# Performance work log

Measured on AMD Instinct MI355X. Metric: run time of the kernel, lower is better.

Reference implementation:

```python
import jax, jax.numpy as jnp
import numpy as np

TAU_MEM, TAU_SYN = 20.0, 5.0
THRESHOLD, BETA, RESET = 1.0, 4.0, 0.0
ALPHA_MEM = float(np.exp(-1.0 / TAU_MEM))
ALPHA_SYN = float(np.exp(-1.0 / TAU_SYN))
EPS = 1e-6


def _lif(x, W, b):
    # x: [B,T,D] -> spikes_with_grad: [B,T,H] (faithful to original incl. the
    # spikes + stop_grad(spikes - surrogate) expression, forward value 2*s - sg)
    cur = jnp.einsum('btd,dh->bth', x, W) + b  # all-timestep projection (same math as per-step dense)
    B, T, H = cur.shape
    v0 = jnp.zeros((B, H), cur.dtype)
    i0 = jnp.zeros((B, H), cur.dtype)

    def step(carry, ic):
        v, i = carry
        i = ALPHA_SYN * i + ic
        v = ALPHA_MEM * v + (1.0 - ALPHA_MEM) * i
        spikes = (v >= THRESHOLD).astype(jnp.float32)
        sg = BETA / (2.0 * (1.0 + jnp.cosh(BETA * (v - THRESHOLD))))
        swg = spikes + jax.lax.stop_gradient(spikes - sg)
        v = jnp.where(spikes > 0, RESET, v)
        return (v, i), swg

    (_, _), out = jax.lax.scan(step, (v0, i0), cur.transpose(1, 0, 2))
    return out.transpose(1, 0, 2)


def _layernorm(x, scale, bias):
    mu = jnp.mean(x, axis=-1, keepdims=True)
    var = jnp.var(x, axis=-1, keepdims=True)
    return (x - mu) * jax.lax.rsqrt(var + EPS) * scale + bias


def setup_inputs() -> dict:
    key = jax.random.key(0)
    ks = jax.random.split(key, 8)
    B, T, D = 512, 128, 512
    H0, H1, H2, C = 256, 128, 64, 2
    s = 0.02
    return {
        'spike_trains': jax.random.uniform(ks[0], (B, T, D), jnp.float32),
        'W0': jax.random.normal(ks[1], (D, H0), jnp.float32) * s,
        'b0': jnp.zeros((H0,), jnp.float32),
        'ln1_scale': jnp.ones((H0,), jnp.float32),
        'ln1_bias': jnp.zeros((H0,), jnp.float32),
        'W1': jax.random.normal(ks[2], (H0, H1), jnp.float32) * s,
        'b1': jnp.zeros((H1,), jnp.float32),
        'ln2_scale': jnp.ones((H1,), jnp.float32),
        'ln2_bias': jnp.zeros((H1,), jnp.float32),
        'W2': jax.random.normal(ks[3], (H1, H2), jnp.float32) * s,
        'b2': jnp.zeros((H2,), jnp.float32),
        'Wc': jax.random.normal(ks[4], (H2, C), jnp.float32) * s,
        'bc': jnp.zeros((C,), jnp.float32),
    }


def reference(spike_trains, W0, b0, ln1_scale, ln1_bias, W1, b1,
              ln2_scale, ln2_bias, W2, b2, Wc, bc):
    x = _lif(spike_trains, W0, b0)                    # layer 0: no pre-norm
    x = _lif(_layernorm(x, ln1_scale, ln1_bias), W1, b1)
    x = _lif(_layernorm(x, ln2_scale, ln2_bias), W2, b2)
    pooled = jnp.mean(x, axis=1)                      # [B, H2]
    logits = pooled @ Wc + bc                         # [B, C]
    return logits, pooled, jnp.mean(x)
```

## Files before the change

kernel.cpp:

```cpp
#include <hip/hip_runtime.h>
#include <cstddef>

static constexpr float A_MEM  = 0.951229424500714f;
static constexpr float A_SYN  = 0.8187307530779818f;
static constexpr float OM_MEM = 0.04877057549928599f;

template<int NT, int K, int H, bool LN, bool POOL>
__global__ __launch_bounds__(NT) void layer_fused(
    const float* __restrict__ A, const float* __restrict__ W,
    const float* __restrict__ bias,
    const float* __restrict__ lns, const float* __restrict__ lnb,
    float* __restrict__ out)
{
  constexpr int T = 128;
  constexpr int BK = 16;
  constexpr int TXB = (NT == 512) ? 5 : 4;
  constexpr int NTX = 1 << TXB;
  constexpr int NJ  = H / NTX;
  constexpr int S   = K / BK;
  constexpr int APT = (BK * 128 / 4) / NT;
  constexpr int WPT = (BK * H / 4) / NT < 1 ? 1 : (BK * H / 4) / NT;
  extern __shared__ __align__(16) float smem[];
  float* As  = smem;
  float* Ws  = smem + BK * 128;
  float* buf = smem;

  const int b   = blockIdx.x;
  const int tid = threadIdx.x;
  const int tx  = tid & (NTX - 1);
  const int ty  = tid >> TXB;
  const float* Ab = A + (size_t)b * T * K;

  float acc[8][NJ];
  #pragma unroll
  for (int i = 0; i < 8; ++i)
    #pragma unroll
    for (int j = 0; j < NJ; ++j) acc[i][j] = 0.f;

  float4 aR[APT], wR[WPT];
  auto load_tile = [&](int k0) {
    #pragma unroll
    for (int p = 0; p < APT; ++p) {
      int f4 = tid + p * NT;
      int r  = f4 >> 2;
      int c4 = (f4 & 3) << 2;
      aR[p] = *(const float4*)(Ab + (size_t)r * K + k0 + c4);
    }
    #pragma unroll
    for (int p = 0; p < WPT; ++p) {
      int f4 = tid + p * NT;
      int k  = f4 / (H / 4);
      int c4 = (f4 % (H / 4)) << 2;
      wR[p] = *(const float4*)(W + (size_t)(k0 + k) * H + c4);
    }
  };

  load_tile(0);
  for (int s = 0; s < S; ++s) {
    __syncthreads();
    #pragma unroll
    for (int p = 0; p < APT; ++p) {
      int f4 = tid + p * NT;
      int r  = f4 >> 2;
      int c4 = (f4 & 3) << 2;
      As[(c4 + 0) * 128 + r] = aR[p].x;
      As[(c4 + 1) * 128 + r] = aR[p].y;
      As[(c4 + 2) * 128 + r] = aR[p].z;
      As[(c4 + 3) * 128 + r] = aR[p].w;
    }
    #pragma unroll
    for (int p = 0; p < WPT; ++p) {
      int f4 = tid + p * NT;
      int k  = f4 / (H / 4);
      int c4 = (f4 % (H / 4)) << 2;
      *(float4*)(Ws + k * H + c4) = wR[p];
    }
    __syncthreads();
    if (s + 1 < S) load_tile((s + 1) * BK);
    #pragma unroll
    for (int kk = 0; kk < BK; ++kk) {
      float4 a0 = *(const float4*)(As + kk * 128 + ty * 8);
      float4 a1 = *(const float4*)(As + kk * 128 + ty * 8 + 4);
      float av[8] = {a0.x, a0.y, a0.z, a0.w, a1.x, a1.y, a1.z, a1.w};
      float bv[NJ];
      #pragma unroll
      for (int j = 0; j < NJ; ++j) bv[j] = Ws[kk * H + j * NTX + tx];
      #pragma unroll
      for (int i = 0; i < 8; ++i)
        #pragma unroll
        for (int j = 0; j < NJ; ++j)
          acc[i][j] += av[i] * bv[j];
    }
  }

  __syncthreads();
  {
    float bb[NJ];
    #pragma unroll
    for (int j = 0; j < NJ; ++j) bb[j] = bias[j * NTX + tx];
    #pragma unroll
    for (int i = 0; i < 8; ++i) {
      int row = ty * 8 + i;
      #pragma unroll
      for (int j = 0; j < NJ; ++j)
        buf[row * H + j * NTX + tx] = acc[i][j] + bb[j];
    }
  }
  __syncthreads();

  if (tid < H) {
    float v = 0.f, cin = 0.f, sum = 0.f;
    for (int t = 0; t < T; ++t) {
      float ic = buf[t * H + tid];
      cin = A_SYN * cin + ic;
      v = A_MEM * v + OM_MEM * cin;
      bool sp = (v >= 1.0f);
      float xx = 4.0f * (v - 1.0f);
      float e  = __expf(xx);
      float tp = 1.0f + e;
      float sg = 4.0f * e / (tp * tp);
      float o  = (sp ? 2.0f : 0.0f) - sg;
      if (POOL) sum += o;
      else buf[t * H + tid] = o;
      v = sp ? 0.0f : v;
    }
    if (POOL) out[(size_t)b * H + tid] = sum * (1.0f / 128.0f);
  }

  if (LN) {
    __syncthreads();
    constexpr int VPL = H / 64;
    constexpr int NW  = NT / 64;
    const int wv   = tid >> 6;
    const int lane = tid & 63;
    float sc[VPL], bi[VPL];
    #pragma unroll
    for (int q = 0; q < VPL; ++q) {
      sc[q] = lns[lane * VPL + q];
      bi[q] = lnb[lane * VPL + q];
    }
    for (int t = wv; t < T; t += NW) {
      float vals[VPL];
      #pragma unroll
      for (int q = 0; q < VPL; ++q) vals[q] = buf[t * H + lane * VPL + q];
      float s1 = 0.f, s2 = 0.f;
      #pragma unroll
      for (int q = 0; q < VPL; ++q) { s1 += vals[q]; s2 += vals[q] * vals[q]; }
      #pragma unroll
      for (int off = 32; off; off >>= 1) {
        s1 += __shfl_xor(s1, off);
        s2 += __shfl_xor(s2, off);
      }
      float mu  = s1 * (1.0f / H);
      float var = s2 * (1.0f / H) - mu * mu;
      float rs  = rsqrtf(var + 1e-6f);
      float* op = out + ((size_t)b * T + t) * H + lane * VPL;
      #pragma unroll
      for (int q = 0; q < VPL; ++q)
        op[q] = (vals[q] - mu) * rs * sc[q] + bi[q];
    }
  }
}

__global__ __launch_bounds__(1024) void head_k(
    const float* __restrict__ pooled, const float* __restrict__ Wc,
    const float* __restrict__ bc, float* __restrict__ logits,
    float* __restrict__ meanp)
{
    const int tid = threadIdx.x;
    const int b = tid >> 1, c = tid & 1;
    float accl = 0.f;
    #pragma unroll 8
    for (int k = 0; k < 64; ++k) accl += pooled[b * 64 + k] * Wc[k * 2 + c];
    logits[tid] = accl + bc[c];

    float s = 0.f;
    for (int i2 = tid; i2 < 512 * 64; i2 += 1024) s += pooled[i2];
    #pragma unroll
    for (int off = 32; off; off >>= 1) s += __shfl_xor(s, off);
    __shared__ float red[16];
    const int wave = tid >> 6, lane = tid & 63;
    if (lane == 0) red[wave] = s;
    __syncthreads();
    if (tid == 0) {
        float tot = 0.f;
        #pragma unroll
        for (int w = 0; w < 16; ++w) tot += red[w];
        meanp[0] = tot * (1.0f / 32768.0f);
    }
}

extern "C" void kernel_launch(void* const* d_in, const int* in_sizes, int n_in,
                              void* d_out, int out_size, void* d_ws, size_t ws_size,
                              hipStream_t stream) {
    const float* x    = (const float*)d_in[0];
    const float* W0   = (const float*)d_in[1];
    const float* b0   = (const float*)d_in[2];
    const float* ln1s = (const float*)d_in[3];
    const float* ln1b = (const float*)d_in[4];
    const float* W1   = (const float*)d_in[5];
    const float* b1   = (const float*)d_in[6];
    const float* ln2s = (const float*)d_in[7];
    const float* ln2b = (const float*)d_in[8];
    const float* W2   = (const float*)d_in[9];
    const float* b2   = (const float*)d_in[10];
    const float* Wc   = (const float*)d_in[11];
    const float* bc   = (const float*)d_in[12];

    float* out    = (float*)d_out;
    float* logits = out;
    float* pooled = out + 1024;
    float* meanp  = out + 1024 + 32768;

    const int B = 512;
    float* y1 = (float*)d_ws;
    float* y2 = y1 + (size_t)65536 * 256;

    (void)hipFuncSetAttribute((const void*)&layer_fused<512,512,256,true,false>,
                              hipFuncAttributeMaxDynamicSharedMemorySize, 131072);
    (void)hipFuncSetAttribute((const void*)&layer_fused<256,256,128,true,false>,
                              hipFuncAttributeMaxDynamicSharedMemorySize, 65536);
    (void)hipFuncSetAttribute((const void*)&layer_fused<256,128,64,false,true>,
                              hipFuncAttributeMaxDynamicSharedMemorySize, 32768);

    layer_fused<512,512,256,true,false><<<B, 512, 131072, stream>>>(
        x,  W0, b0, ln1s, ln1b, y1);
    layer_fused<256,256,128,true,false><<<B, 256, 65536, stream>>>(
        y1, W1, b1, ln2s, ln2b, y2);
    layer_fused<256,128,64,false,true><<<B, 256, 32768, stream>>>(
        y2, W2, b2, nullptr, nullptr, pooled);
    head_k<<<1, 1024, 0, stream>>>(pooled, Wc, bc, logits, meanp);
}
```

Baseline: 639.5 us.

## Split fused layers into tiled GEMM, LIF-stats and pooled LIF kernels

Replaces the one-block-per-batch fused layer kernel with separate GEMM kernels using smaller row tiles (more blocks), a LIF scan kernel that writes spikes in place and computes per-timestep layernorm mean/rstd, and the next GEMM applying layernorm on the fly while loading A. The aim is to stop the LIF scan from serialising only H threads inside a large-shared-memory block, and to raise occupancy for the GEMM. In exchange, the pre-activation currents make extra round trips through global memory and there are more kernel launches.

```diff
diff --git a/kernel.cpp b/kernel.cpp
--- a/kernel.cpp
+++ b/kernel.cpp
@@ -5,161 +5,205 @@
 static constexpr float A_SYN  = 0.8187307530779818f;
 static constexpr float OM_MEM = 0.04877057549928599f;
 
-template<int NT, int K, int H, bool LN, bool POOL>
-__global__ __launch_bounds__(NT) void layer_fused(
+template<int BM, int BN, int K, bool LN>
+__global__ __launch_bounds__(256) void gemm_ln(
     const float* __restrict__ A, const float* __restrict__ W,
     const float* __restrict__ bias,
-    const float* __restrict__ lns, const float* __restrict__ lnb,
-    float* __restrict__ out)
-{
-  constexpr int T = 128;
-  constexpr int BK = 16;
-  constexpr int TXB = (NT == 512) ? 5 : 4;
-  constexpr int NTX = 1 << TXB;
-  constexpr int NJ  = H / NTX;
-  constexpr int S   = K / BK;
-  constexpr int APT = (BK * 128 / 4) / NT;
-  constexpr int WPT = (BK * H / 4) / NT < 1 ? 1 : (BK * H / 4) / NT;
-  extern __shared__ __align__(16) float smem[];
-  float* As  = smem;
-  float* Ws  = smem + BK * 128;
-  float* buf = smem;
-
-  const int b   = blockIdx.x;
+    const float2* __restrict__ stats, const float* __restrict__ lnsc,
+    const float* __restrict__ lnbi, float* __restrict__ C)
+{
+  constexpr int BK   = 16;
+  constexpr int S    = K / BK;
+  constexpr int PA   = BM + 4;
+  constexpr int NTYG = BM / 8;
+  constexpr int NTX  = 256 / NTYG;
+  constexpr int CJ   = BN / (NTX * 2);
+  constexpr int APT  = BM / 64;
+  constexpr int WPT  = BN / 64;
+
+  __shared__ float As[BK][PA];
+  __shared__ float Ws[BK][BN];
+
   const int tid = threadIdx.x;
-  const int tx  = tid & (NTX - 1);
-  const int ty  = tid >> TXB;
-  const float* Ab = A + (size_t)b * T * K;
-
-  float acc[8][NJ];
+  const int tx  = tid % NTX;
+  const int ty  = tid / NTX;
+  const int m0  = blockIdx.x * BM;
+
+  float4 aR[APT], wR[WPT];
+
+  auto load_tile = [&](int k0) {
+    #pragma unroll
+    for (int p = 0; p < APT; ++p) {
+      int idx = tid + p * 256;
+      int r = idx >> 2, c4 = (idx & 3) << 2;
+      float4 a = *(const float4*)(A + (size_t)(m0 + r) * K + k0 + c4);
+      if constexpr (LN) {
+        float2 st = stats[m0 + r];
+        float4 ls = *(const float4*)(lnsc + k0 + c4);
+        float4 lb = *(const float4*)(lnbi + k0 + c4);
+        a.x = (a.x - st.x) * st.y * ls.x + lb.x;
+        a.y = (a.y - st.x) * st.y * ls.y + lb.y;
+        a.z = (a.z - st.x) * st.y * ls.z + lb.z;
+        a.w = (a.w - st.x) * st.y * ls.w + lb.w;
+      }
+      aR[p] = a;
+    }
+    #pragma unroll
+    for (int p = 0; p < WPT; ++p) {
+      int idx = tid + p * 256;
+      int k = idx / (BN / 4), c4 = (idx % (BN / 4)) << 2;
+      wR[p] = *(const float4*)(W + (size_t)(k0 + k) * BN + c4);
+    }
+  };
+
+  auto store_tile = [&]() {
+    #pragma unroll
+    for (int p = 0; p < APT; ++p) {
+      int idx = tid + p * 256;
+      int r = idx >> 2, c4 = (idx & 3) << 2;
+      As[c4 + 0][r] = aR[p].x;
+      As[c4 + 1][r] = aR[p].y;
+      As[c4 + 2][r] = aR[p].z;
+      As[c4 + 3][r] = aR[p].w;
+    }
+    #pragma unroll
+    for (int p = 0; p < WPT; ++p) {
+      int idx = tid + p * 256;
+      int k = idx / (BN / 4), c4 = (idx % (BN / 4)) << 2;
+      *(float4*)&Ws[k][c4] = wR[p];
+    }
+  };
+
+  float acc[8][CJ * 2];
   #pragma unroll
   for (int i = 0; i < 8; ++i)
     #pragma unroll
-    for (int j = 0; j < NJ; ++j) acc[i][j] = 0.f;
-
-  float4 aR[APT], wR[WPT];
-  auto load_tile = [&](int k0) {
-    #pragma unroll
-    for (int p = 0; p < APT; ++p) {
-      int f4 = tid + p * NT;
-      int r  = f4 >> 2;
-      int c4 = (f4 & 3) << 2;
-      aR[p] = *(const float4*)(Ab + (size_t)r * K + k0 + c4);
-    }
-    #pragma unroll
-    for (int p = 0; p < WPT; ++p) {
-      int f4 = tid + p * NT;
-      int k  = f4 / (H / 4);
-      int c4 = (f4 % (H / 4)) << 2;
-      wR[p] = *(const float4*)(W + (size_t)(k0 + k) * H + c4);
-    }
-  };
+    for (int j = 0; j < CJ * 2; ++j) acc[i][j] = 0.f;
 
   load_tile(0);
   for (int s = 0; s < S; ++s) {
     __syncthreads();
-    #pragma unroll
-    for (int p = 0; p < APT; ++p) {
-      int f4 = tid + p * NT;
-      int r  = f4 >> 2;
-      int c4 = (f4 & 3) << 2;
-      As[(c4 + 0) * 128 + r] = aR[p].x;
-      As[(c4 + 1) * 128 + r] = aR[p].y;
-      As[(c4 + 2) * 128 + r] = aR[p].z;
-      As[(c4 + 3) * 128 + r] = aR[p].w;
-    }
-    #pragma unroll
-    for (int p = 0; p < WPT; ++p) {
-      int f4 = tid + p * NT;
-      int k  = f4 / (H / 4);
-      int c4 = (f4 % (H / 4)) << 2;
-      *(float4*)(Ws + k * H + c4) = wR[p];
-    }
+    store_tile();
     __syncthreads();
     if (s + 1 < S) load_tile((s + 1) * BK);
     #pragma unroll
     for (int kk = 0; kk < BK; ++kk) {
-      float4 a0 = *(const float4*)(As + kk * 128 + ty * 8);
-      float4 a1 = *(const float4*)(As + kk * 128 + ty * 8 + 4);
+      float4 a0 = *(const float4*)&As[kk][ty * 8];
+      float4 a1 = *(const float4*)&As[kk][ty * 8 + 4];
       float av[8] = {a0.x, a0.y, a0.z, a0.w, a1.x, a1.y, a1.z, a1.w};
-      float bv[NJ];
+      float2 wv[CJ];
       #pragma unroll
-      for (int j = 0; j < NJ; ++j) bv[j] = Ws[kk * H + j * NTX + tx];
+      for (int j = 0; j < CJ; ++j)
+        wv[j] = *(const float2*)&Ws[kk][tx * 2 + j * NTX * 2];
       #pragma unroll
       for (int i = 0; i < 8; ++i)
         #pragma unroll
-        for (int j = 0; j < NJ; ++j)
-          acc[i][j] += av[i] * bv[j];
-    }
-  }
-
-  __syncthreads();
-  {
-    float bb[NJ];
-    #pragma unroll
-    for (int j = 0; j < NJ; ++j) bb[j] = bias[j * NTX + tx];
+        for (int j = 0; j < CJ; ++j) {
+          acc[i][2 * j]     += av[i] * wv[j].x;
+          acc[i][2 * j + 1] += av[i] * wv[j].y;
+        }
+    }
+  }
+
+  #pragma unroll
+  for (int j = 0; j < CJ; ++j) {
+    int col = tx * 2 + j * NTX * 2;
+    float2 bb = *(const float2*)(bias + col);
     #pragma unroll
     for (int i = 0; i < 8; ++i) {
-      int row = ty * 8 + i;
-      #pragma unroll
-      for (int j = 0; j < NJ; ++j)
-        buf[row * H + j * NTX + tx] = acc[i][j] + bb[j];
-    }
-  }
-  __syncthreads();
-
-  if (tid < H) {
-    float v = 0.f, cin = 0.f, sum = 0.f;
-    for (int t = 0; t < T; ++t) {
-      float ic = buf[t * H + tid];
-      cin = A_SYN * cin + ic;
-      v = A_MEM * v + OM_MEM * cin;
-      bool sp = (v >= 1.0f);
+      int row = m0 + ty * 8 + i;
+      float2 o;
+      o.x = acc[i][2 * j]     + bb.x;
+      o.y = acc[i][2 * j + 1] + bb.y;
+      *(float2*)(C + (size_t)row * BN + col) = o;
+    }
+  }
+}
+
+template<int H, int BPB>
+__global__ __launch_bounds__(256) void lif_stats(
+    float* __restrict__ cur, float2* __restrict__ stats)
+{
+  constexpr int T = 128;
+  constexpr int WPB = H / 64;
+  const int tid  = threadIdx.x;
+  const int bl   = tid / H;
+  const int h    = tid % H;
+  const size_t b = (size_t)blockIdx.x * BPB + bl;
+  float* p = cur + b * T * H + h;
+  __shared__ float w1[4][T], w2[4][T];
+  const int wv = tid >> 6, lane = tid & 63;
+  float v = 0.f, ci = 0.f;
+  for (int t0 = 0; t0 < T; t0 += 4) {
+    float ic[4];
+    #pragma unroll
+    for (int u = 0; u < 4; ++u) ic[u] = p[(size_t)(t0 + u) * H];
+    #pragma unroll
+    for (int u = 0; u < 4; ++u) {
+      ci = A_SYN * ci + ic[u];
+      v  = A_MEM * v + OM_MEM * ci;
+      bool sp = v >= 1.0f;
       float xx = 4.0f * (v - 1.0f);
       float e  = __expf(xx);
       float tp = 1.0f + e;
       float sg = 4.0f * e / (tp * tp);
       float o  = (sp ? 2.0f : 0.0f) - sg;
-      if (POOL) sum += o;
-      else buf[t * H + tid] = o;
       v = sp ? 0.0f : v;
-    }
-    if (POOL) out[(size_t)b * H + tid] = sum * (1.0f / 128.0f);
-  }
-
-  if (LN) {
-    __syncthreads();
-    constexpr int VPL = H / 64;
-    constexpr int NW  = NT / 64;
-    const int wv   = tid >> 6;
-    const int lane = tid & 63;
-    float sc[VPL], bi[VPL];
-    #pragma unroll
-    for (int q = 0; q < VPL; ++q) {
-      sc[q] = lns[lane * VPL + q];
-      bi[q] = lnb[lane * VPL + q];
-    }
-    for (int t = wv; t < T; t += NW) {
-      float vals[VPL];
+      ic[u] = o;
+      float s1 = o, s2 = o * o;
       #pragma unroll
-      for (int q = 0; q < VPL; ++q) vals[q] = buf[t * H + lane * VPL + q];
-      float s1 = 0.f, s2 = 0.f;
-      #pragma unroll
-      for (int q = 0; q < VPL; ++q) { s1 += vals[q]; s2 += vals[q] * vals[q]; }
-      #pragma unroll
-      for (int off = 32; off; off >>= 1) {
+      for (int off = 1; off < 64; off <<= 1) {
         s1 += __shfl_xor(s1, off);
         s2 += __shfl_xor(s2, off);
       }
-      float mu  = s1 * (1.0f / H);
-      float var = s2 * (1.0f / H) - mu * mu;
-      float rs  = rsqrtf(var + 1e-6f);
-      float* op = out + ((size_t)b * T + t) * H + lane * VPL;
-      #pragma unroll
-      for (int q = 0; q < VPL; ++q)
-        op[q] = (vals[q] - mu) * rs * sc[q] + bi[q];
-    }
-  }
+      if (lane == 0) { w1[wv][t0 + u] = s1; w2[wv][t0 + u] = s2; }
+    }
+    #pragma unroll
+    for (int u = 0; u < 4; ++u) p[(size_t)(t0 + u) * H] = ic[u];
+  }
+  __syncthreads();
+  if (tid < T * BPB) {
+    int t  = tid & (T - 1);
+    int bs = tid >> 7;
+    float s1 = 0.f, s2 = 0.f;
+    #pragma unroll
+    for (int w = 0; w < WPB; ++w) {
+      s1 += w1[bs * WPB + w][t];
+      s2 += w2[bs * WPB + w][t];
+    }
+    float mu  = s1 * (1.0f / H);
+    float var = s2 * (1.0f / H) - mu * mu;
+    float rs  = rsqrtf(var + 1e-6f);
+    stats[((size_t)blockIdx.x * BPB + bs) * T + t] = make_float2(mu, rs);
+  }
+}
+
+__global__ __launch_bounds__(256) void lif_pool(
+    const float* __restrict__ cur, float* __restrict__ pooled)
+{
+  constexpr int T = 128, H = 64;
+  int flat = blockIdx.x * 256 + threadIdx.x;
+  int b = flat >> 6, h = flat & 63;
+  const float* p = cur + (size_t)b * T * H + h;
+  float v = 0.f, ci = 0.f, sum = 0.f;
+  for (int t0 = 0; t0 < T; t0 += 4) {
+    float ic[4];
+    #pragma unroll
+    for (int u = 0; u < 4; ++u) ic[u] = p[(size_t)(t0 + u) * H];
+    #pragma unroll
+    for (int u = 0; u < 4; ++u) {
+      ci = A_SYN * ci + ic[u];
+      v  = A_MEM * v + OM_MEM * ci;
+      bool sp = v >= 1.0f;
+      float xx = 4.0f * (v - 1.0f);
+      float e  = __expf(xx);
+      float tp = 1.0f + e;
+      float sg = 4.0f * e / (tp * tp);
+      sum += (sp ? 2.0f : 0.0f) - sg;
+      v = sp ? 0.0f : v;
+    }
+  }
+  pooled[flat] = sum * (1.0f / 128.0f);
 }
 
 __global__ __launch_bounds__(1024) void head_k(
@@ -167,67 +211,66 @@
     const float* __restrict__ bc, float* __restrict__ logits,
     float* __restrict__ meanp)
 {
-    const int tid = threadIdx.x;
-    const int b = tid >> 1, c = tid & 1;
-    float accl = 0.f;
-    #pragma unroll 8
-    for (int k = 0; k < 64; ++k) accl += pooled[b * 64 + k] * Wc[k * 2 + c];
-    logits[tid] = accl + bc[c];
-
-    float s = 0.f;
-    for (int i2 = tid; i2 < 512 * 64; i2 += 1024) s += pooled[i2];
-    #pragma unroll
-    for (int off = 32; off; off >>= 1) s += __shfl_xor(s, off);
-    __shared__ float red[16];
-    const int wave = tid >> 6, lane = tid & 63;
-    if (lane == 0) red[wave] = s;
-    __syncthreads();
-    if (tid == 0) {
-        float tot = 0.f;
-        #pragma unroll
-        for (int w = 0; w < 16; ++w) tot += red[w];
-        meanp[0] = tot * (1.0f / 32768.0f);
-    }
+  const int tid = threadIdx.x;
+  const int b = tid >> 1, c = tid & 1;
+  float accl = 0.f;
+  #pragma unroll 8
+  for (int k = 0; k < 64; ++k) accl += pooled[b * 64 + k] * Wc[k * 2 + c];
+  logits[tid] = accl + bc[c];
+
+  float s = 0.f;
+  for (int i2 = tid; i2 < 512 * 64; i2 += 1024) s += pooled[i2];
+  #pragma unroll
+  for (int off = 32; off; off >>= 1) s += __shfl_xor(s, off);
+  __shared__ float red[16];
+  const int wave = tid >> 6, lane = tid & 63;
+  if (lane == 0) red[wave] = s;
+  __syncthreads();
+  if (tid == 0) {
+    float tot = 0.f;
+    #pragma unroll
+    for (int w = 0; w < 16; ++w) tot += red[w];
+    meanp[0] = tot * (1.0f / 32768.0f);
+  }
 }
 
 extern "C" void kernel_launch(void* const* d_in, const int* in_sizes, int n_in,
                               void* d_out, int out_size, void* d_ws, size_t ws_size,
                               hipStream_t stream) {
-    const float* x    = (const float*)d_in[0];
-    const float* W0   = (const float*)d_in[1];
-    const float* b0   = (const float*)d_in[2];
-    const float* ln1s = (const float*)d_in[3];
-    const float* ln1b = (const float*)d_in[4];
-    const float* W1   = (const float*)d_in[5];
-    const float* b1   = (const float*)d_in[6];
-    const float* ln2s = (const float*)d_in[7];
-    const float* ln2b = (const float*)d_in[8];
-    const float* W2   = (const float*)d_in[9];
-    const float* b2   = (const float*)d_in[10];
-    const float* Wc   = (const float*)d_in[11];
-    const float* bc   = (const float*)d_in[12];
-
-    float* out    = (float*)d_out;
-    float* logits = out;
-    float* pooled = out + 1024;
-    float* meanp  = out + 1024 + 32768;
-
-    const int B = 512;
-    float* y1 = (float*)d_ws;
-    float* y2 = y1 + (size_t)65536 * 256;
-
-    (void)hipFuncSetAttribute((const void*)&layer_fused<512,512,256,true,false>,
-                              hipFuncAttributeMaxDynamicSharedMemorySize, 131072);
-    (void)hipFuncSetAttribute((const void*)&layer_fused<256,256,128,true,false>,
-                              hipFuncAttributeMaxDynamicSharedMemorySize, 65536);
-    (void)hipFuncSetAttribute((const void*)&layer_fused<256,128,64,false,true>,
-                              hipFuncAttributeMaxDynamicSharedMemorySize, 32768);
-
-    layer_fused<512,512,256,true,false><<<B, 512, 131072, stream>>>(
-        x,  W0, b0, ln1s, ln1b, y1);
-    layer_fused<256,256,128,true,false><<<B, 256, 65536, stream>>>(
-        y1, W1, b1, ln2s, ln2b, y2);
-    layer_fused<256,128,64,false,true><<<B, 256, 32768, stream>>>(
-        y2, W2, b2, nullptr, nullptr, pooled);
-    head_k<<<1, 1024, 0, stream>>>(pooled, Wc, bc, logits, meanp);
-}
+  const float* x    = (const float*)d_in[0];
+  const float* W0   = (const float*)d_in[1];
+  const float* b0   = (const float*)d_in[2];
+  const float* ln1s = (const float*)d_in[3];
+  const float* ln1b = (const float*)d_in[4];
+  const float* W1   = (const float*)d_in[5];
+  const float* b1   = (const float*)d_in[6];
+  const float* ln2s = (const float*)d_in[7];
+  const float* ln2b = (const float*)d_in[8];
+  const float* W2   = (const float*)d_in[9];
+  const float* b2   = (const float*)d_in[10];
+  const float* Wc   = (const float*)d_in[11];
+  const float* bc   = (const float*)d_in[12];
+
+  float* out    = (float*)d_out;
+  float* logits = out;
+  float* pooled = out + 1024;
+  float* meanp  = out + 1024 + 32768;
+
+  char* ws = (char*)d_ws;
+  float*  cur0   = (float*)ws;
+  float*  cur1   = (float*)(ws + (size_t)64 * 1024 * 1024);
+  float*  cur2   = (float*)(ws + (size_t)96 * 1024 * 1024);
+  float2* stats0 = (float2*)(ws + (size_t)112 * 1024 * 1024);
+  float2* stats1 = (float2*)(ws + (size_t)112 * 1024 * 1024 + 524288);
+
+  gemm_ln<64, 256, 512, false><<<1024, 256, 0, stream>>>(
+      x, W0, b0, nullptr, nullptr, nullptr, cur0);
+  lif_stats<256, 1><<<512, 256, 0, stream>>>(cur0, stats0);
+  gemm_ln<64, 128, 256, true><<<1024, 256, 0, stream>>>(
+      cur0, W1, b1, stats0, ln1s, ln1b, cur1);
+  lif_stats<128, 2><<<256, 256, 0, stream>>>(cur1, stats1);
+  gemm_ln<128, 64, 128, true><<<512, 256, 0, stream>>>(
+      cur1, W2, b2, stats1, ln2s, ln2b, cur2);
+  lif_pool<<<128, 256, 0, stream>>>(cur2, pooled);
+  head_k<<<1, 1024, 0, stream>>>(pooled, Wc, bc, logits, meanp);
+}
```

New measurement: 623.5 us. 2.5% less time.
